# Kernel optimization log

Measured on AMD Instinct MI355X. Metric: run time of the kernel, lower is better.

## Reference

```python
import jax, jax.numpy as jnp
import numpy as np

B, S, IN, H, OUT, L = 64, 512, 512, 1024, 512, 2


def setup_inputs() -> dict:
    key = jax.random.key(0)
    ks = jax.random.split(key, 12)
    s_in = 1.0 / np.sqrt(IN)
    s_h = 1.0 / np.sqrt(H)
    inp = {
        "x": jax.random.normal(ks[0], (B, S, IN), dtype=jnp.float32),
        "h0": jnp.zeros((B, L, H), dtype=jnp.float32),
        # layer 0: gates stacked [z; r; g] along first axis
        "Wx0": jax.random.uniform(ks[1], (3 * H, IN), minval=-s_in, maxval=s_in),
        "Wh0": jax.random.uniform(ks[2], (3 * H, H), minval=-s_h, maxval=s_h),
        "bh0": jax.random.uniform(ks[3], (3 * H,), minval=-s_h, maxval=s_h),
        # layer 1 (input dim is H)
        "Wx1": jax.random.uniform(ks[4], (3 * H, H), minval=-s_h, maxval=s_h),
        "Wh1": jax.random.uniform(ks[5], (3 * H, H), minval=-s_h, maxval=s_h),
        "bh1": jax.random.uniform(ks[6], (3 * H,), minval=-s_h, maxval=s_h),
        # output projection fc_hy
        "Why": jax.random.uniform(ks[7], (OUT, H), minval=-s_h, maxval=s_h),
        "by": jax.random.uniform(ks[8], (OUT,), minval=-s_h, maxval=s_h),
    }
    return inp


def _gru_layer(x, h_init, Wx, Wh, bh):
    """x: [B,S,D], h_init: [B,H]. Returns (ys [B,S,H], h_final [B,H])."""
    # Batch the input-side projections for all timesteps at once.
    xp = jnp.einsum("bsd,gd->bsg", x, Wx)  # [B,S,3H]
    xz, xr, xg = jnp.split(xp, 3, axis=-1)
    Whz, Whr, Whg = jnp.split(Wh, 3, axis=0)
    bhz, bhr, bhg = jnp.split(bh, 3, axis=0)

    def step(h, xs):
        xz_t, xr_t, xg_t = xs  # each [B,H]
        z = jax.nn.sigmoid(xz_t + h @ Whz.T + bhz)
        r = jax.nn.sigmoid(xr_t + h @ Whr.T + bhr)
        g = jnp.tanh(xg_t + (r * h) @ Whg.T + bhg)
        h_new = z * h + (1.0 - z) * g
        return h_new, h_new

    # time-major scan
    xs = (xz.transpose(1, 0, 2), xr.transpose(1, 0, 2), xg.transpose(1, 0, 2))
    h_final, ys = jax.lax.scan(step, h_init, xs)
    return ys.transpose(1, 0, 2), h_final  # [B,S,H], [B,H]


def reference(x, h0, Wx0, Wh0, bh0, Wx1, Wh1, bh1, Why, by):
    # dropout rate is 0 -> dropout is identity
    y0, hf0 = _gru_layer(x, h0[:, 0, :], Wx0, Wh0, bh0)
    y1, hf1 = _gru_layer(y0, h0[:, 1, :], Wx1, Wh1, bh1)
    layer_output = jnp.einsum("bsh,oh->bso", y1, Why) + by  # [B,S,OUT]
    hidden_state = jnp.stack([hf0, hf1], axis=1)  # [B,L,H]
    return layer_output, jax.lax.stop_gradient(hidden_state)
```

## Files before the change

### kernel.cpp

```cpp
#include <hip/hip_runtime.h>
#include <hip/hip_bf16.h>

#define B_   64
#define S_   512
#define IN_  512
#define H_   1024
#define OUT_ 512
#define H3_  3072
#define TC_  32
#define TCL2 5
#define NCHUNK (S_ / TC_)
#define MC_  (B_ * TC_)
#define NROW (B_ * S_)

#define NBLK 128
#define NTHR 512
#define EXN  32768
#define FPAD 16
#define STAGE_OFF 0
#define HOWN_OFF  32768
#define ZOWN_OFF  36928
#define SMEM_BYTES 41088

typedef float f32x4 __attribute__((ext_vector_type(4)));
typedef short bf16x8 __attribute__((ext_vector_type(8)));
typedef unsigned int u32;
typedef u32 u32x4 __attribute__((ext_vector_type(4)));

struct ChainArgs {
  const float* xp;
  const __hip_bfloat16* Wh;
  float* hf;
  u32* hbuf;
  u32* rhbuf;
  u32* fA;
  u32* fB;
  __hip_bfloat16* y;
  u32 baseA, baseB;
  int t0;
  int layer;
  int active;
  int stagger;
};

__device__ __forceinline__ u32 f2bf_bits(float v) {
  union { __hip_bfloat16 b; unsigned short s; } cv;
  cv.b = __float2bfloat16(v);
  return (u32)cv.s;
}

__device__ __forceinline__ void coh_st(u32* p, u32 v) {
  __hip_atomic_store(p, v, __ATOMIC_RELAXED, __HIP_MEMORY_SCOPE_AGENT);
}
__device__ __forceinline__ u32 coh_ld(const u32* p) {
  return __hip_atomic_load(p, __ATOMIC_RELAXED, __HIP_MEMORY_SCOPE_AGENT);
}

__device__ __forceinline__ void waitflags(const u32* f, int rgbase, u32 target) {
  const u32* my = f + (size_t)(rgbase + (threadIdx.x & 15)) * FPAD;
  int it = 0;
  while (true) {
    u32 v = coh_ld(my);
    if (__all((int)(v >= target))) break;
    if (it < 2) {
      __builtin_amdgcn_s_sleep(2);
    } else {
      __builtin_amdgcn_s_sleep(8);
    }
    ++it;
  }
  __builtin_amdgcn_sched_barrier(0);
}

__device__ __forceinline__ void stage_ex(const u32* __restrict__ src, char* stage, int tid,
                                         int rg) {
  u32x4 v[4];
#pragma unroll
  for (int i = 0; i < 4; ++i) {
    int c4 = tid + i * NTHR;
    int cgp = c4 >> 7;
    int s = c4 & 127;
    const u32* p = src + (((size_t)(cgp * 4 + rg) * 16 + (s >> 3)) * 32 + (s & 7) * 4);
    asm volatile("global_load_dwordx4 %0, %1, off sc0 sc1" : "=v"(v[i]) : "v"(p));
  }
  asm volatile("s_waitcnt vmcnt(0)" ::: "memory");
#pragma unroll
  for (int i = 0; i < 4; ++i) {
    int c4 = tid + i * NTHR;
    int cgp = c4 >> 7;
    int s = c4 & 127;
    int r = s >> 3;
    *(u32x4*)(stage + r * 2048 + ((cgp * 128 + (s & 7) * 16) ^ ((r & 7) << 4))) = v[i];
  }
}

__global__ __launch_bounds__(256) void cast_f32_to_bf16(const float* __restrict__ in,
                                                        __hip_bfloat16* __restrict__ out,
                                                        int n4) {
  int i = blockIdx.x * 256 + threadIdx.x;
  if (i >= n4) return;
  float4 v = ((const float4*)in)[i];
  out[4 * i + 0] = __float2bfloat16(v.x);
  out[4 * i + 1] = __float2bfloat16(v.y);
  out[4 * i + 2] = __float2bfloat16(v.z);
  out[4 * i + 3] = __float2bfloat16(v.w);
}

__global__ __launch_bounds__(256) void gather_cast_x(const float* __restrict__ x,
                                                     __hip_bfloat16* __restrict__ out, int t0) {
  int i = blockIdx.x * 256 + threadIdx.x;
  int e = i * 4;
  int b = e >> 14;
  int rem = e & 16383;
  float4 v = *(const float4*)(x + (size_t)b * (S_ * IN_) + (size_t)t0 * IN_ + rem);
  out[e + 0] = __float2bfloat16(v.x);
  out[e + 1] = __float2bfloat16(v.y);
  out[e + 2] = __float2bfloat16(v.z);
  out[e + 3] = __float2bfloat16(v.w);
}

template <bool REMAP>
__global__ __launch_bounds__(256) void gemm_nt_bias(const __hip_bfloat16* __restrict__ A,
                                                    const __hip_bfloat16* __restrict__ Bm,
                                                    const float* __restrict__ bias,
                                                    float* __restrict__ C, int M, int N, int K,
                                                    int t0) {
  const int lane = threadIdx.x & 63;
  const int w = threadIdx.x >> 6;
  const int wr = w >> 1, wc = w & 1;
  const int row0 = blockIdx.y * 128 + wr * 64;
  const int col0 = blockIdx.x * 128 + wc * 64;
  const int kl = (lane >> 4) * 8;
  const int m16 = lane & 15;
  f32x4 acc[4][4] = {};
  for (int k0 = 0; k0 < K; k0 += 32) {
    bf16x8 a[4], b[4];
#pragma unroll
    for (int i = 0; i < 4; ++i)
      a[i] = *(const bf16x8*)(A + (size_t)(row0 + i * 16 + m16) * K + k0 + kl);
#pragma unroll
    for (int j = 0; j < 4; ++j)
      b[j] = *(const bf16x8*)(Bm + (size_t)(col0 + j * 16 + m16) * K + k0 + kl);
#pragma unroll
    for (int i = 0; i < 4; ++i)
#pragma unroll
      for (int j = 0; j < 4; ++j)
        acc[i][j] = __builtin_amdgcn_mfma_f32_16x16x32_bf16(a[i], b[j], acc[i][j], 0, 0, 0);
  }
  const int rsub = (lane >> 4) * 4;
#pragma unroll
  for (int i = 0; i < 4; ++i) {
    int row = row0 + i * 16 + rsub;
#pragma unroll
    for (int j = 0; j < 4; ++j) {
      int col = col0 + j * 16 + m16;
      float bv = bias[col];
#pragma unroll
      for (int r = 0; r < 4; ++r) {
        int rr = row + r;
        int crow = REMAP ? ((rr >> TCL2) * S_ + t0 + (rr & (TC_ - 1))) : rr;
        C[(size_t)crow * N + col] = acc[i][j][r] + bv;
      }
    }
  }
}

__device__ __forceinline__ void chain_scan(const ChainArgs& ca, const float* __restrict__ h0,
                                           float* __restrict__ hid_out, char* smem, int bx) {
  char* stage = smem + STAGE_OFF;
  float* h_own = (float*)(smem + HOWN_OFF);
  float* z_own = (float*)(smem + ZOWN_OFF);

  const int tid = threadIdx.x;
  const int lane = tid & 63;
  const int w = tid >> 6;
  const int wc = w & 3;
  const int isR = w >> 2;
  const int rg = bx >> 4;
  const int cg = bx & 15;
  const int fid = bx;
  const int rgbase = rg * 16;
  const int m16 = lane & 15;
  const int kl = (lane >> 4) * 8;
  const int rsub = (lane >> 4) * 4;
  const int swzA = (m16 & 7) << 4;
  const int cloc = wc * 16 + m16;

  const float* xp = ca.xp;
  const __hip_bfloat16* Wh = ca.Wh;
  u32* hbuf = ca.hbuf;
  u32* rhbuf = ca.rhbuf;
  u32* flagA = ca.fA;
  u32* flagB = ca.fB;
  const u32 baseA = ca.baseA, baseB = ca.baseB;
  const int t0 = ca.t0, layer = ca.layer;

  for (int i = 0; i < ca.stagger; ++i) __builtin_amdgcn_s_sleep(16);

  {
    int row = tid >> 5, pp = tid & 31;
    int col = cg * 64 + pp * 2;
    int grow = rg * 16 + row;
    float v0, v1;
    if (t0 == 0) {
      v0 = h0[((size_t)grow * 2 + layer) * H_ + col];
      v1 = h0[((size_t)grow * 2 + layer) * H_ + col + 1];
      coh_st(hbuf + EXN + (((size_t)(cg * 4 + rg) * 16 + row) * 32 + pp),
             f2bf_bits(v0) | (f2bf_bits(v1) << 16));
    } else {
      v0 = ca.hf[grow * H_ + col];
      v1 = ca.hf[grow * H_ + col + 1];
    }
    h_own[row * 65 + pp * 2] = v0;
    h_own[row * 65 + pp * 2 + 1] = v1;
  }
  asm volatile("s_waitcnt vmcnt(0)" ::: "memory");
  __syncthreads();
  if (tid == 0) coh_st(flagB + (size_t)fid * FPAD, baseB + 1);

  for (int t = 0; t < TC_; ++t) {
    const int par = t & 1;
    const int colA = cg * 64 + cloc + (isR ? H_ : 0);
    float xpv[4], xpg[4];
#pragma unroll
    for (int j = 0; j < 4; ++j) {
      int grow = rg * 16 + rsub + j;
      xpv[j] = xp[((size_t)(grow * TC_ + t)) * H3_ + colA];
    }
    if (w < 4) {
#pragma unroll
      for (int j = 0; j < 4; ++j) {
        int grow = rg * 16 + rsub + j;
        xpg[j] = xp[((size_t)(grow * TC_ + t)) * H3_ + 2 * H_ + cg * 64 + cloc];
      }
    }

    waitflags(flagB, rgbase, baseB + 1 + t);
    stage_ex(hbuf + (par ^ 1) * EXN, stage, tid, rg);
    __syncthreads();
    {
      f32x4 acc0 = {}, acc1 = {};
      const char* abase = stage + m16 * 2048;
      const __hip_bfloat16* Bb = Wh + (size_t)colA * H_;
#pragma unroll
      for (int k0 = 0; k0 < H_; k0 += 64) {
        bf16x8 a0 = *(const bf16x8*)(abase + (((k0 + kl) * 2) ^ swzA));
        bf16x8 a1 = *(const bf16x8*)(abase + (((k0 + 32 + kl) * 2) ^ swzA));
        bf16x8 b0 = *(const bf16x8*)(Bb + k0 + kl);
        bf16x8 b1 = *(const bf16x8*)(Bb + k0 + 32 + kl);
        acc0 = __builtin_amdgcn_mfma_f32_16x16x32_bf16(a0, b0, acc0, 0, 0, 0);
        acc1 = __builtin_amdgcn_mfma_f32_16x16x32_bf16(a1, b1, acc1, 0, 0, 0);
      }
      if (!isR) {
#pragma unroll
        for (int j = 0; j < 4; ++j) {
          float pre = acc0[j] + acc1[j] + xpv[j];
          z_own[(rsub + j) * 65 + cloc] = 1.f / (1.f + expf(-pre));
        }
      } else {
#pragma unroll
        for (int j = 0; j < 4; ++j) {
          int lr = rsub + j;
          float pre = acc0[j] + acc1[j] + xpv[j];
          float s = 1.f / (1.f + expf(-pre));
          float rh = s * h_own[lr * 65 + cloc];
          u32 bits = f2bf_bits(rh);
          u32 pair = bits | (((u32)__shfl_down((int)bits, 1)) << 16);
          if ((m16 & 1) == 0)
            coh_st(rhbuf + par * EXN + (((size_t)(cg * 4 + rg) * 16 + lr) * 32 + (cloc >> 1)),
                   pair);
        }
        asm volatile("s_waitcnt vmcnt(0)" ::: "memory");
      }
    }
    __syncthreads();
    if (tid == 0) coh_st(flagA + (size_t)fid * FPAD, baseA + t + 1);

    waitflags(flagA, rgbase, baseA + t + 1);
    stage_ex(rhbuf + par * EXN, stage, tid, rg);
    __syncthreads();
    if (w < 4) {
      f32x4 acc0 = {}, acc1 = {};
      const char* abase = stage + m16 * 2048;
      const __hip_bfloat16* Bb = Wh + (size_t)(2 * H_ + cg * 64 + cloc) * H_;
#pragma unroll
      for (int k0 = 0; k0 < H_; k0 += 64) {
        bf16x8 a0 = *(const bf16x8*)(abase + (((k0 + kl) * 2) ^ swzA));
        bf16x8 a1 = *(const bf16x8*)(abase + (((k0 + 32 + kl) * 2) ^ swzA));
        bf16x8 b0 = *(const bf16x8*)(Bb + k0 + kl);
        bf16x8 b1 = *(const bf16x8*)(Bb + k0 + 32 + kl);
        acc0 = __builtin_amdgcn_mfma_f32_16x16x32_bf16(a0, b0, acc0, 0, 0, 0);
        acc1 = __builtin_amdgcn_mfma_f32_16x16x32_bf16(a1, b1, acc1, 0, 0, 0);
      }
#pragma unroll
      for (int j = 0; j < 4; ++j) {
        int lr = rsub + j;
        float pre = acc0[j] + acc1[j] + xpg[j];
        float gg = tanhf(pre);
        float zz = z_own[lr * 65 + cloc];
        float hv = h_own[lr * 65 + cloc];
        float hn = zz * hv + (1.f - zz) * gg;
        h_own[lr * 65 + cloc] = hn;
        u32 bits = f2bf_bits(hn);
        u32 pair = bits | (((u32)__shfl_down((int)bits, 1)) << 16);
        if ((m16 & 1) == 0)
          coh_st(hbuf + par * EXN + (((size_t)(cg * 4 + rg) * 16 + lr) * 32 + (cloc >> 1)), pair);
        ca.y[((size_t)((rg * 16 + lr) * TC_ + t)) * H_ + cg * 64 + cloc] = __float2bfloat16(hn);
      }
      asm volatile("s_waitcnt vmcnt(0)" ::: "memory");
    }
    __syncthreads();
    if (tid == 0) coh_st(flagB + (size_t)fid * FPAD, baseB + t + 2);
  }

  {
    int row = tid >> 5, pp = tid & 31;
    int col = cg * 64 + pp * 2;
    int grow = rg * 16 + row;
    float v0 = h_own[row * 65 + pp * 2];
    float v1 = h_own[row * 65 + pp * 2 + 1];
    ca.hf[grow * H_ + col] = v0;
    ca.hf[grow * H_ + col + 1] = v1;
    if (t0 + TC_ == S_) {
      hid_out[((size_t)grow * 2 + layer) * H_ + col] = v0;
      hid_out[((size_t)grow * 2 + layer) * H_ + col + 1] = v1;
    }
  }
}

__global__ __launch_bounds__(NTHR) void gru_scan_fused(ChainArgs a0, ChainArgs a1,
                                                       const float* __restrict__ h0,
                                                       float* __restrict__ hid_out) {
  extern __shared__ char smem[];
  if (blockIdx.x < 64) {
    if (!a0.active) return;
    chain_scan(a0, h0, hid_out, smem, blockIdx.x);
  } else {
    if (!a1.active) return;
    chain_scan(a1, h0, hid_out, smem, blockIdx.x - 64);
  }
}

extern "C" void kernel_launch(void* const* d_in, const int* in_sizes, int n_in,
                              void* d_out, int out_size, void* d_ws, size_t ws_size,
                              hipStream_t stream) {
  const float* x   = (const float*)d_in[0];
  const float* h0  = (const float*)d_in[1];
  const float* Wx0 = (const float*)d_in[2];
  const float* Wh0 = (const float*)d_in[3];
  const float* bh0 = (const float*)d_in[4];
  const float* Wx1 = (const float*)d_in[5];
  const float* Wh1 = (const float*)d_in[6];
  const float* bh1 = (const float*)d_in[7];
  const float* Why = (const float*)d_in[8];
  const float* by  = (const float*)d_in[9];
  float* out = (float*)d_out;
  float* hid_out = out + (size_t)NROW * OUT_;

  (void)hipFuncSetAttribute((const void*)gru_scan_fused,
                            hipFuncAttributeMaxDynamicSharedMemorySize, SMEM_BYTES);

  char* ws = (char*)d_ws;
  size_t off = 0;
  auto alloc = [&](size_t bytes) {
    char* p = ws + off;
    off += (bytes + 255) & ~(size_t)255;
    return p;
  };
  __hip_bfloat16* wx0b = (__hip_bfloat16*)alloc((size_t)H3_ * IN_ * 2);
  __hip_bfloat16* wh0b = (__hip_bfloat16*)alloc((size_t)H3_ * H_ * 2);
  __hip_bfloat16* wx1b = (__hip_bfloat16*)alloc((size_t)H3_ * H_ * 2);
  __hip_bfloat16* wh1b = (__hip_bfloat16*)alloc((size_t)H3_ * H_ * 2);
  __hip_bfloat16* whyb = (__hip_bfloat16*)alloc((size_t)OUT_ * H_ * 2);
  float* h_f32_0 = (float*)alloc((size_t)B_ * H_ * 4);
  float* h_f32_1 = (float*)alloc((size_t)B_ * H_ * 4);
  u32* hbuf_0  = (u32*)alloc((size_t)2 * EXN * 4);
  u32* hbuf_1  = (u32*)alloc((size_t)2 * EXN * 4);
  u32* rhbuf_0 = (u32*)alloc((size_t)2 * EXN * 4);
  u32* rhbuf_1 = (u32*)alloc((size_t)2 * EXN * 4);
  __hip_bfloat16* x_bfc = (__hip_bfloat16*)alloc((size_t)MC_ * IN_ * 2);
  __hip_bfloat16* y0buf = (__hip_bfloat16*)alloc((size_t)MC_ * H_ * 2);
  __hip_bfloat16* y1buf = (__hip_bfloat16*)alloc((size_t)MC_ * H_ * 2);
  float* xp0buf = (float*)alloc((size_t)MC_ * H3_ * 4);
  float* xp1buf = (float*)alloc((size_t)MC_ * H3_ * 4);
  u32* flags    = (u32*)alloc(4 * 256 * FPAD * 4);
  (void)ws_size;

  (void)hipMemsetAsync(flags, 0, 4 * 256 * FPAD * 4, stream);

  auto cast = [&](const float* in, __hip_bfloat16* o, size_t n) {
    cast_f32_to_bf16<<<dim3((unsigned)((n / 4 + 255) / 256)), dim3(256), 0, stream>>>(in, o,
                                                                                     (int)(n / 4));
  };
  cast(Wx0, wx0b, (size_t)H3_ * IN_);
  cast(Wh0, wh0b, (size_t)H3_ * H_);
  cast(Wx1, wx1b, (size_t)H3_ * H_);
  cast(Wh1, wh1b, (size_t)H3_ * H_);
  cast(Why, whyb, (size_t)OUT_ * H_);

  u32* fA0 = flags;
  u32* fB0 = flags + 256 * FPAD;
  u32* fA1 = flags + 512 * FPAD;
  u32* fB1 = flags + 768 * FPAD;

  auto mkchain = [&](int layer, int chunk, int active) {
    ChainArgs ca;
    int cc = chunk < 0 ? 0 : chunk;
    ca.xp = layer == 0 ? xp0buf : xp1buf;
    ca.Wh = layer == 0 ? wh0b : wh1b;
    ca.hf = layer == 0 ? h_f32_0 : h_f32_1;
    ca.hbuf = layer == 0 ? hbuf_0 : hbuf_1;
    ca.rhbuf = layer == 0 ? rhbuf_0 : rhbuf_1;
    ca.fA = layer == 0 ? fA0 : fA1;
    ca.fB = layer == 0 ? fB0 : fB1;
    ca.y = layer == 0 ? y0buf : y1buf;
    ca.baseA = (u32)cc * TC_;
    ca.baseB = (u32)cc * (TC_ + 1);
    ca.t0 = cc * TC_;
    ca.layer = layer;
    ca.active = active;
    ca.stagger = (layer == 1) ? 14 : 0;
    return ca;
  };

  gather_cast_x<<<dim3(MC_ * IN_ / 4 / 256), dim3(256), 0, stream>>>(x, x_bfc, 0);
  gemm_nt_bias<false><<<dim3(H3_ / 128, MC_ / 128), dim3(256), 0, stream>>>(
      x_bfc, wx0b, bh0, xp0buf, MC_, H3_, IN_, 0);

  for (int c = 0; c <= NCHUNK; ++c) {
    ChainArgs a0 = mkchain(0, c, c < NCHUNK ? 1 : 0);
    ChainArgs a1 = mkchain(1, c - 1, c > 0 ? 1 : 0);
    {
      void* args[] = {(void*)&a0, (void*)&a1, (void*)&h0, (void*)&hid_out};
      hipError_t e = hipLaunchCooperativeKernel((void*)gru_scan_fused, dim3(NBLK), dim3(NTHR),
                                                args, SMEM_BYTES, stream);
      if (e != hipSuccess) {
        (void)hipGetLastError();
        gru_scan_fused<<<dim3(NBLK), dim3(NTHR), SMEM_BYTES, stream>>>(a0, a1, h0, hid_out);
      }
    }
    if (c < NCHUNK) {
      gemm_nt_bias<false><<<dim3(H3_ / 128, MC_ / 128), dim3(256), 0, stream>>>(
          y0buf, wx1b, bh1, xp1buf, MC_, H3_, H_, 0);
    }
    if (c + 1 < NCHUNK) {
      gather_cast_x<<<dim3(MC_ * IN_ / 4 / 256), dim3(256), 0, stream>>>(x, x_bfc, (c + 1) * TC_);
      gemm_nt_bias<false><<<dim3(H3_ / 128, MC_ / 128), dim3(256), 0, stream>>>(
          x_bfc, wx0b, bh0, xp0buf, MC_, H3_, IN_, 0);
    }
    if (c > 0) {
      gemm_nt_bias<true><<<dim3(OUT_ / 128, MC_ / 128), dim3(256), 0, stream>>>(
          y1buf, whyb, by, out, MC_, OUT_, H_, (c - 1) * TC_);
    }
  }
}
```

Measured before the change: 10.82 ms.

## Run next-chunk input projection and output GEMM on spare blocks inside scan kernel

The persistent scan kernel grows from 128 to 256 blocks. The extra 128 blocks compute the next chunk's layer-0 input projection, casting x to bf16 inline, and the output projection of the chunk before last while the recurrent chains run. The xp0 and y1 buffers are double-buffered so this overlapped work does not clash with the scan's reads and writes, and the separate per-chunk GEMM launches are removed, with one final output GEMM left after the loop. The flag polling also changes to an inline-asm global load with sc0 sc1 bits. Risks: the GEMM blocks may compete with the latency-bound scan blocks for CUs and memory bandwidth, and the cooperative launch must still fit 256 blocks.

```diff
diff --git a/kernel.cpp b/kernel.cpp
--- a/kernel.cpp
+++ b/kernel.cpp
@@ -13,7 +13,7 @@
 #define MC_  (B_ * TC_)
 #define NROW (B_ * S_)
 
-#define NBLK 128
+#define NBLK 256
 #define NTHR 512
 #define EXN  32768
 #define FPAD 16
@@ -43,6 +43,21 @@
   int stagger;
 };
 
+struct GemmTasks {
+  const float* x;
+  const __hip_bfloat16* wx0;
+  const float* bh0;
+  float* xp0dst;
+  int t0next;
+  int xp0_active;
+  const __hip_bfloat16* y1src;
+  const __hip_bfloat16* why;
+  const float* by;
+  float* outdst;
+  int t0out;
+  int out_active;
+};
+
 __device__ __forceinline__ u32 f2bf_bits(float v) {
   union { __hip_bfloat16 b; unsigned short s; } cv;
   cv.b = __float2bfloat16(v);
@@ -52,15 +67,14 @@
 __device__ __forceinline__ void coh_st(u32* p, u32 v) {
   __hip_atomic_store(p, v, __ATOMIC_RELAXED, __HIP_MEMORY_SCOPE_AGENT);
 }
-__device__ __forceinline__ u32 coh_ld(const u32* p) {
-  return __hip_atomic_load(p, __ATOMIC_RELAXED, __HIP_MEMORY_SCOPE_AGENT);
-}
 
 __device__ __forceinline__ void waitflags(const u32* f, int rgbase, u32 target) {
   const u32* my = f + (size_t)(rgbase + (threadIdx.x & 15)) * FPAD;
   int it = 0;
   while (true) {
-    u32 v = coh_ld(my);
+    u32 v;
+    asm volatile("global_load_dword %0, %1, off sc0 sc1\n\ts_waitcnt vmcnt(0)"
+                 : "=v"(v) : "v"(my) : "memory");
     if (__all((int)(v >= target))) break;
     if (it < 2) {
       __builtin_amdgcn_s_sleep(2);
@@ -165,8 +179,115 @@
   }
 }
 
-__device__ __forceinline__ void chain_scan(const ChainArgs& ca, const float* __restrict__ h0,
-                                           float* __restrict__ hid_out, char* smem, int bx) {
+__device__ void xp0_unit(const GemmTasks& gt, int u, int tl) {
+  const int lane = tl & 63;
+  const int w = tl >> 6;
+  const int wr = w >> 1, wc = w & 1;
+  const int row0 = (u & 15) * 128 + wr * 64;
+  const int col0 = (u >> 4) * 128 + wc * 64;
+  const int kl = (lane >> 4) * 8;
+  const int m16 = lane & 15;
+  f32x4 acc[4][4] = {};
+  for (int k0 = 0; k0 < IN_; k0 += 32) {
+    bf16x8 a[4], b[4];
+#pragma unroll
+    for (int i = 0; i < 4; ++i) {
+      int rr = row0 + i * 16 + m16;
+      int xrow = (rr >> TCL2) * S_ + gt.t0next + (rr & (TC_ - 1));
+      const float* ap = gt.x + (size_t)xrow * IN_ + k0 + kl;
+      float4 f0 = *(const float4*)ap;
+      float4 f1 = *(const float4*)(ap + 4);
+      union { unsigned short s[8]; bf16x8 v; } cv;
+      cv.s[0] = (unsigned short)f2bf_bits(f0.x);
+      cv.s[1] = (unsigned short)f2bf_bits(f0.y);
+      cv.s[2] = (unsigned short)f2bf_bits(f0.z);
+      cv.s[3] = (unsigned short)f2bf_bits(f0.w);
+      cv.s[4] = (unsigned short)f2bf_bits(f1.x);
+      cv.s[5] = (unsigned short)f2bf_bits(f1.y);
+      cv.s[6] = (unsigned short)f2bf_bits(f1.z);
+      cv.s[7] = (unsigned short)f2bf_bits(f1.w);
+      a[i] = cv.v;
+    }
+#pragma unroll
+    for (int j = 0; j < 4; ++j)
+      b[j] = *(const bf16x8*)(gt.wx0 + (size_t)(col0 + j * 16 + m16) * IN_ + k0 + kl);
+#pragma unroll
+    for (int i = 0; i < 4; ++i)
+#pragma unroll
+      for (int j = 0; j < 4; ++j)
+        acc[i][j] = __builtin_amdgcn_mfma_f32_16x16x32_bf16(a[i], b[j], acc[i][j], 0, 0, 0);
+  }
+  const int rsub = (lane >> 4) * 4;
+#pragma unroll
+  for (int i = 0; i < 4; ++i) {
+    int row = row0 + i * 16 + rsub;
+#pragma unroll
+    for (int j = 0; j < 4; ++j) {
+      int col = col0 + j * 16 + m16;
+      float bv = gt.bh0[col];
+#pragma unroll
+      for (int r = 0; r < 4; ++r)
+        gt.xp0dst[(size_t)(row + r) * H3_ + col] = acc[i][j][r] + bv;
+    }
+  }
+}
+
+__device__ void out_unit(const GemmTasks& gt, int u, int tl) {
+  const int lane = tl & 63;
+  const int w = tl >> 6;
+  const int wr = w >> 1, wc = w & 1;
+  const int row0 = (u & 15) * 128 + wr * 64;
+  const int col0 = (u >> 4) * 128 + wc * 64;
+  const int kl = (lane >> 4) * 8;
+  const int m16 = lane & 15;
+  f32x4 acc[4][4] = {};
+  for (int k0 = 0; k0 < H_; k0 += 32) {
+    bf16x8 a[4], b[4];
+#pragma unroll
+    for (int i = 0; i < 4; ++i)
+      a[i] = *(const bf16x8*)(gt.y1src + (size_t)(row0 + i * 16 + m16) * H_ + k0 + kl);
+#pragma unroll
+    for (int j = 0; j < 4; ++j)
+      b[j] = *(const bf16x8*)(gt.why + (size_t)(col0 + j * 16 + m16) * H_ + k0 + kl);
+#pragma unroll
+    for (int i = 0; i < 4; ++i)
+#pragma unroll
+      for (int j = 0; j < 4; ++j)
+        acc[i][j] = __builtin_amdgcn_mfma_f32_16x16x32_bf16(a[i], b[j], acc[i][j], 0, 0, 0);
+  }
+  const int rsub = (lane >> 4) * 4;
+#pragma unroll
+  for (int i = 0; i < 4; ++i) {
+    int row = row0 + i * 16 + rsub;
+#pragma unroll
+    for (int j = 0; j < 4; ++j) {
+      int col = col0 + j * 16 + m16;
+      float bv = gt.by[col];
+#pragma unroll
+      for (int r = 0; r < 4; ++r) {
+        int rr = row + r;
+        int crow = (rr >> TCL2) * S_ + gt.t0out + (rr & (TC_ - 1));
+        gt.outdst[(size_t)crow * OUT_ + col] = acc[i][j][r] + bv;
+      }
+    }
+  }
+}
+
+__device__ void gemm_spare(const GemmTasks& gt) {
+  const int gb = (int)blockIdx.x - 128;
+  const int h = threadIdx.x >> 8;
+  const int tl = threadIdx.x & 255;
+  for (int u = gb * 2 + h; u < 448; u += 256) {
+    if (u < 384) {
+      if (gt.xp0_active) xp0_unit(gt, u, tl);
+    } else {
+      if (gt.out_active) out_unit(gt, u - 384, tl);
+    }
+  }
+}
+
+__device__ void chain_scan(const ChainArgs& ca, const float* __restrict__ h0,
+                           float* __restrict__ hid_out, char* smem, int bx) {
   char* stage = smem + STAGE_OFF;
   float* h_own = (float*)(smem + HOWN_OFF);
   float* z_own = (float*)(smem + ZOWN_OFF);
@@ -330,14 +451,18 @@
 
 __global__ __launch_bounds__(NTHR) void gru_scan_fused(ChainArgs a0, ChainArgs a1,
                                                        const float* __restrict__ h0,
-                                                       float* __restrict__ hid_out) {
+                                                       float* __restrict__ hid_out,
+                                                       GemmTasks gt) {
   extern __shared__ char smem[];
-  if (blockIdx.x < 64) {
+  const int bx = blockIdx.x;
+  if (bx < 64) {
     if (!a0.active) return;
-    chain_scan(a0, h0, hid_out, smem, blockIdx.x);
+    chain_scan(a0, h0, hid_out, smem, bx);
+  } else if (bx < 128) {
+    if (!a1.active) return;
+    chain_scan(a1, h0, hid_out, smem, bx - 64);
   } else {
-    if (!a1.active) return;
-    chain_scan(a1, h0, hid_out, smem, blockIdx.x - 64);
+    gemm_spare(gt);
   }
 }
 
@@ -380,10 +505,12 @@
   u32* rhbuf_1 = (u32*)alloc((size_t)2 * EXN * 4);
   __hip_bfloat16* x_bfc = (__hip_bfloat16*)alloc((size_t)MC_ * IN_ * 2);
   __hip_bfloat16* y0buf = (__hip_bfloat16*)alloc((size_t)MC_ * H_ * 2);
-  __hip_bfloat16* y1buf = (__hip_bfloat16*)alloc((size_t)MC_ * H_ * 2);
-  float* xp0buf = (float*)alloc((size_t)MC_ * H3_ * 4);
-  float* xp1buf = (float*)alloc((size_t)MC_ * H3_ * 4);
-  u32* flags    = (u32*)alloc(4 * 256 * FPAD * 4);
+  __hip_bfloat16* y1buf0 = (__hip_bfloat16*)alloc((size_t)MC_ * H_ * 2);
+  __hip_bfloat16* y1buf1 = (__hip_bfloat16*)alloc((size_t)MC_ * H_ * 2);
+  float* xp0buf0 = (float*)alloc((size_t)MC_ * H3_ * 4);
+  float* xp0buf1 = (float*)alloc((size_t)MC_ * H3_ * 4);
+  float* xp1buf  = (float*)alloc((size_t)MC_ * H3_ * 4);
+  u32* flags     = (u32*)alloc(4 * 256 * FPAD * 4);
   (void)ws_size;
 
   (void)hipMemsetAsync(flags, 0, 4 * 256 * FPAD * 4, stream);
@@ -402,18 +529,20 @@
   u32* fB0 = flags + 256 * FPAD;
   u32* fA1 = flags + 512 * FPAD;
   u32* fB1 = flags + 768 * FPAD;
+  float* xp0bufs[2] = {xp0buf0, xp0buf1};
+  __hip_bfloat16* y1bufs[2] = {y1buf0, y1buf1};
 
   auto mkchain = [&](int layer, int chunk, int active) {
     ChainArgs ca;
     int cc = chunk < 0 ? 0 : chunk;
-    ca.xp = layer == 0 ? xp0buf : xp1buf;
+    ca.xp = layer == 0 ? xp0bufs[cc & 1] : xp1buf;
     ca.Wh = layer == 0 ? wh0b : wh1b;
     ca.hf = layer == 0 ? h_f32_0 : h_f32_1;
     ca.hbuf = layer == 0 ? hbuf_0 : hbuf_1;
     ca.rhbuf = layer == 0 ? rhbuf_0 : rhbuf_1;
     ca.fA = layer == 0 ? fA0 : fA1;
     ca.fB = layer == 0 ? fB0 : fB1;
-    ca.y = layer == 0 ? y0buf : y1buf;
+    ca.y = layer == 0 ? y0buf : y1bufs[cc & 1];
     ca.baseA = (u32)cc * TC_;
     ca.baseB = (u32)cc * (TC_ + 1);
     ca.t0 = cc * TC_;
@@ -425,32 +554,38 @@
 
   gather_cast_x<<<dim3(MC_ * IN_ / 4 / 256), dim3(256), 0, stream>>>(x, x_bfc, 0);
   gemm_nt_bias<false><<<dim3(H3_ / 128, MC_ / 128), dim3(256), 0, stream>>>(
-      x_bfc, wx0b, bh0, xp0buf, MC_, H3_, IN_, 0);
+      x_bfc, wx0b, bh0, xp0buf0, MC_, H3_, IN_, 0);
 
   for (int c = 0; c <= NCHUNK; ++c) {
     ChainArgs a0 = mkchain(0, c, c < NCHUNK ? 1 : 0);
     ChainArgs a1 = mkchain(1, c - 1, c > 0 ? 1 : 0);
+    GemmTasks gt;
+    gt.x = x;
+    gt.wx0 = wx0b;
+    gt.bh0 = bh0;
+    gt.xp0dst = xp0bufs[(c + 1) & 1];
+    gt.t0next = (c + 1) * TC_;
+    gt.xp0_active = (c + 1 < NCHUNK) ? 1 : 0;
+    gt.y1src = y1bufs[c & 1];
+    gt.why = whyb;
+    gt.by = by;
+    gt.outdst = out;
+    gt.t0out = (c - 2) * TC_;
+    gt.out_active = (c >= 2) ? 1 : 0;
     {
-      void* args[] = {(void*)&a0, (void*)&a1, (void*)&h0, (void*)&hid_out};
+      void* args[] = {(void*)&a0, (void*)&a1, (void*)&h0, (void*)&hid_out, (void*)&gt};
       hipError_t e = hipLaunchCooperativeKernel((void*)gru_scan_fused, dim3(NBLK), dim3(NTHR),
                                                 args, SMEM_BYTES, stream);
       if (e != hipSuccess) {
         (void)hipGetLastError();
-        gru_scan_fused<<<dim3(NBLK), dim3(NTHR), SMEM_BYTES, stream>>>(a0, a1, h0, hid_out);
+        gru_scan_fused<<<dim3(NBLK), dim3(NTHR), SMEM_BYTES, stream>>>(a0, a1, h0, hid_out, gt);
       }
     }
     if (c < NCHUNK) {
       gemm_nt_bias<false><<<dim3(H3_ / 128, MC_ / 128), dim3(256), 0, stream>>>(
           y0buf, wx1b, bh1, xp1buf, MC_, H3_, H_, 0);
     }
-    if (c + 1 < NCHUNK) {
-      gather_cast_x<<<dim3(MC_ * IN_ / 4 / 256), dim3(256), 0, stream>>>(x, x_bfc, (c + 1) * TC_);
-      gemm_nt_bias<false><<<dim3(H3_ / 128, MC_ / 128), dim3(256), 0, stream>>>(
-          x_bfc, wx0b, bh0, xp0buf, MC_, H3_, IN_, 0);
-    }
-    if (c > 0) {
-      gemm_nt_bias<true><<<dim3(OUT_ / 128, MC_ / 128), dim3(256), 0, stream>>>(
-          y1buf, whyb, by, out, MC_, OUT_, H_, (c - 1) * TC_);
-    }
-  }
-}
+  }
+  gemm_nt_bias<true><<<dim3(OUT_ / 128, MC_ / 128), dim3(256), 0, stream>>>(
+      y1bufs[(NCHUNK - 1) & 1], whyb, by, out, MC_, OUT_, H_, (NCHUNK - 1) * TC_);
+}
```

Measured after the change: 9.840 ms, median of 3. -9.1%, faster.
